# Performance work log

Measured on AMD Instinct MI355X. Metric: run time of the kernel, lower is better.

The kernel has to match this reference:

```python
import jax, jax.numpy as jnp
import numpy as np

EPS = 1e-12  # matches torch F.normalize default eps
WEIGHT = jnp.array([1.0, 1.0, 1.0], dtype=jnp.float32)  # per-channel loss weights


def _l2norm(x, axis):
    # torch F.normalize: x / max(||x||_2, eps)
    n = jnp.sqrt(jnp.sum(x * x, axis=axis, keepdims=True))
    return x / jnp.maximum(n, EPS)


def setup_inputs() -> dict:
    key = jax.random.key(0)
    k1, k2 = jax.random.split(key)
    shape = (16, 3, 512, 512)  # [B, C, H, W]
    return {
        "x": jax.random.normal(k1, shape, dtype=jnp.float32),
        "ref": jax.random.normal(k2, shape, dtype=jnp.float32),
    }


def reference(x, ref):
    # trace(rownorm(A) @ rownorm(B)^T) == sum(rownorm(A) * rownorm(B));
    # trace(colnorm(A)^T @ colnorm(B)) == sum(colnorm(A) * colnorm(B)).
    B, C, H, W = x.shape
    # per (batch, channel) traces, vectorized over all dims
    a = jnp.sum(_l2norm(x, -1) * _l2norm(ref, -1), axis=(-2, -1)) / H  # [B, C]
    b = jnp.sum(_l2norm(x, -2) * _l2norm(ref, -2), axis=(-2, -1)) / W  # [B, C]
    a = -jnp.sum(a * WEIGHT) / B
    b = -jnp.sum(b * WEIGHT) / B
    return a + b
```

## Files before the change

### kernel.cpp

```cpp
#include <hip/hip_runtime.h>

#define B_N 16
#define C_N 3
#define H_N 512
#define W_N 512
#define PLANES (B_N * C_N)
#define ROWS_PER_BLOCK 32
#define CHUNKS (H_N / ROWS_PER_BLOCK)
#define NBLK (PLANES * CHUNKS)
#define STATS3 (W_N * 3)
#define SCALE (-1.0f / 8192.0f)
#define EPS_F 1e-12f

__global__ __launch_bounds__(256) void spl_main_kernel(
    const float* __restrict__ x, const float* __restrict__ r,
    float* __restrict__ colpart, float* __restrict__ rowpart) {
    const int p     = blockIdx.x / CHUNKS;
    const int chunk = blockIdx.x % CHUNKS;
    const int wave  = threadIdx.x >> 6;
    const int lane  = threadIdx.x & 63;

    const float* xp = x + (size_t)p * (H_N * W_N);
    const float* rp = r + (size_t)p * (H_N * W_N);

    float cxx[8] = {0, 0, 0, 0, 0, 0, 0, 0};
    float crr[8] = {0, 0, 0, 0, 0, 0, 0, 0};
    float cxr[8] = {0, 0, 0, 0, 0, 0, 0, 0};
    float rowacc = 0.0f;

    const int r0 = chunk * ROWS_PER_BLOCK;
    for (int j = 0; j < ROWS_PER_BLOCK / 4; ++j) {
        const int row = r0 + wave + 4 * j;
        const float4* xr4 = (const float4*)(xp + (size_t)row * W_N);
        const float4* rr4 = (const float4*)(rp + (size_t)row * W_N);
        const float4 xa = xr4[lane];
        const float4 xb = xr4[lane + 64];
        const float4 ra = rr4[lane];
        const float4 rb = rr4[lane + 64];

        cxx[0] += xa.x * xa.x; cxx[1] += xa.y * xa.y; cxx[2] += xa.z * xa.z; cxx[3] += xa.w * xa.w;
        cxx[4] += xb.x * xb.x; cxx[5] += xb.y * xb.y; cxx[6] += xb.z * xb.z; cxx[7] += xb.w * xb.w;
        crr[0] += ra.x * ra.x; crr[1] += ra.y * ra.y; crr[2] += ra.z * ra.z; crr[3] += ra.w * ra.w;
        crr[4] += rb.x * rb.x; crr[5] += rb.y * rb.y; crr[6] += rb.z * rb.z; crr[7] += rb.w * rb.w;
        cxr[0] += xa.x * ra.x; cxr[1] += xa.y * ra.y; cxr[2] += xa.z * ra.z; cxr[3] += xa.w * ra.w;
        cxr[4] += xb.x * rb.x; cxr[5] += xb.y * rb.y; cxr[6] += xb.z * rb.z; cxr[7] += xb.w * rb.w;

        float sxx = cxx[0] + cxx[1] + cxx[2] + cxx[3] + cxx[4] + cxx[5] + cxx[6] + cxx[7];
        float srr = crr[0] + crr[1] + crr[2] + crr[3] + crr[4] + crr[5] + crr[6] + crr[7];
        float sxr = cxr[0] + cxr[1] + cxr[2] + cxr[3] + cxr[4] + cxr[5] + cxr[6] + cxr[7];
        sxx = xa.x * xa.x + xa.y * xa.y + xa.z * xa.z + xa.w * xa.w
            + xb.x * xb.x + xb.y * xb.y + xb.z * xb.z + xb.w * xb.w;
        srr = ra.x * ra.x + ra.y * ra.y + ra.z * ra.z + ra.w * ra.w
            + rb.x * rb.x + rb.y * rb.y + rb.z * rb.z + rb.w * rb.w;
        sxr = xa.x * ra.x + xa.y * ra.y + xa.z * ra.z + xa.w * ra.w
            + xb.x * rb.x + xb.y * rb.y + xb.z * rb.z + xb.w * rb.w;
        #pragma unroll
        for (int m = 32; m > 0; m >>= 1) {
            sxx += __shfl_down(sxx, m, 64);
            srr += __shfl_down(srr, m, 64);
            sxr += __shfl_down(sxr, m, 64);
        }
        if (lane == 0) {
            const float nx = fmaxf(sqrtf(sxx), EPS_F);
            const float nr = fmaxf(sqrtf(srr), EPS_F);
            rowacc += sxr / (nx * nr);
        }
    }

    __shared__ float smem[4][STATS3];
    #pragma unroll
    for (int k = 0; k < 4; ++k) {
        const int c0 = 4 * lane + k;
        const int c1 = c0 + 256;
        smem[wave][c0 * 3 + 0] = cxx[k];
        smem[wave][c0 * 3 + 1] = crr[k];
        smem[wave][c0 * 3 + 2] = cxr[k];
        smem[wave][c1 * 3 + 0] = cxx[4 + k];
        smem[wave][c1 * 3 + 1] = crr[4 + k];
        smem[wave][c1 * 3 + 2] = cxr[4 + k];
    }
    __shared__ float rowsums[4];
    if (lane == 0) rowsums[wave] = rowacc;
    __syncthreads();

    float* cp = colpart + (size_t)blockIdx.x * STATS3;
    #pragma unroll
    for (int k = 0; k < 6; ++k) {
        const int e = threadIdx.x + 256 * k;
        cp[e] = smem[0][e] + smem[1][e] + smem[2][e] + smem[3][e];
    }
    if (threadIdx.x == 0)
        rowpart[blockIdx.x] = rowsums[0] + rowsums[1] + rowsums[2] + rowsums[3];
}

__global__ __launch_bounds__(256) void spl_reduce_kernel(
    const float* __restrict__ colpart, const float* __restrict__ rowpart,
    float* __restrict__ planesum) {
    const int p = blockIdx.x;
    float acc[6] = {0, 0, 0, 0, 0, 0};
    const float* base = colpart + (size_t)p * CHUNKS * STATS3;
    for (int c = 0; c < CHUNKS; ++c) {
        const float* bc = base + c * STATS3;
        #pragma unroll
        for (int k = 0; k < 6; ++k) acc[k] += bc[threadIdx.x + 256 * k];
    }
    __shared__ float sums[STATS3];
    #pragma unroll
    for (int k = 0; k < 6; ++k) sums[threadIdx.x + 256 * k] = acc[k];
    __syncthreads();

    float term = 0.0f;
    #pragma unroll
    for (int k = 0; k < 2; ++k) {
        const int col = threadIdx.x + 256 * k;
        const float sxx = sums[col * 3 + 0];
        const float srr = sums[col * 3 + 1];
        const float sxr = sums[col * 3 + 2];
        term += sxr / (fmaxf(sqrtf(sxx), EPS_F) * fmaxf(sqrtf(srr), EPS_F));
    }
    if (threadIdx.x < CHUNKS) term += rowpart[p * CHUNKS + threadIdx.x];

    #pragma unroll
    for (int m = 32; m > 0; m >>= 1) term += __shfl_down(term, m, 64);
    __shared__ float ws[4];
    if ((threadIdx.x & 63) == 0) ws[threadIdx.x >> 6] = term;
    __syncthreads();
    if (threadIdx.x == 0) planesum[p] = ws[0] + ws[1] + ws[2] + ws[3];
}

__global__ void spl_final_kernel(const float* __restrict__ planesum,
                                 float* __restrict__ out) {
    float v = (threadIdx.x < PLANES) ? planesum[threadIdx.x] : 0.0f;
    #pragma unroll
    for (int m = 32; m > 0; m >>= 1) v += __shfl_down(v, m, 64);
    if (threadIdx.x == 0) out[0] = SCALE * v;
}

extern "C" void kernel_launch(void* const* d_in, const int* in_sizes, int n_in,
                              void* d_out, int out_size, void* d_ws, size_t ws_size,
                              hipStream_t stream) {
    const float* x   = (const float*)d_in[0];
    const float* ref = (const float*)d_in[1];
    float* out = (float*)d_out;

    float* colpart  = (float*)d_ws;
    float* rowpart  = colpart + (size_t)NBLK * STATS3;
    float* planesum = rowpart + NBLK;

    spl_main_kernel<<<NBLK, 256, 0, stream>>>(x, ref, colpart, rowpart);
    spl_reduce_kernel<<<PLANES, 256, 0, stream>>>(colpart, rowpart, planesum);
    spl_final_kernel<<<1, 64, 0, stream>>>(planesum, out);
}
```

Before: 119.9 us.

## Batch row reductions per wave and halve rows per block for more parallelism

Each wave now handles four consecutive rows with a fully unrolled loop, so all loads are issued up front. The cross-lane shuffle reductions for the four rows are interleaved after the loads instead of running after every row. Rows per block drop from 32 to 16, which doubles the block count and the colpart traffic written and read by the reduce kernel. The launch bound now asks for 6 blocks per SIMD, which may constrain registers.

Result: slower. 188.3 us (+57.0%).

```diff
diff --git a/kernel.cpp b/kernel.cpp
--- a/kernel.cpp
+++ b/kernel.cpp
@@ -5,14 +5,15 @@
 #define H_N 512
 #define W_N 512
 #define PLANES (B_N * C_N)
-#define ROWS_PER_BLOCK 32
+#define ROWS_PER_BLOCK 16
+#define ROWS_PER_WAVE 4
 #define CHUNKS (H_N / ROWS_PER_BLOCK)
 #define NBLK (PLANES * CHUNKS)
 #define STATS3 (W_N * 3)
 #define SCALE (-1.0f / 8192.0f)
 #define EPS_F 1e-12f
 
-__global__ __launch_bounds__(256) void spl_main_kernel(
+__global__ __launch_bounds__(256, 6) void spl_main_kernel(
     const float* __restrict__ x, const float* __restrict__ r,
     float* __restrict__ colpart, float* __restrict__ rowpart) {
     const int p     = blockIdx.x / CHUNKS;
@@ -26,11 +27,12 @@
     float cxx[8] = {0, 0, 0, 0, 0, 0, 0, 0};
     float crr[8] = {0, 0, 0, 0, 0, 0, 0, 0};
     float cxr[8] = {0, 0, 0, 0, 0, 0, 0, 0};
-    float rowacc = 0.0f;
+    float psxx[ROWS_PER_WAVE], psrr[ROWS_PER_WAVE], psxr[ROWS_PER_WAVE];
 
-    const int r0 = chunk * ROWS_PER_BLOCK;
-    for (int j = 0; j < ROWS_PER_BLOCK / 4; ++j) {
-        const int row = r0 + wave + 4 * j;
+    const int r0 = chunk * ROWS_PER_BLOCK + wave * ROWS_PER_WAVE;
+    #pragma unroll
+    for (int j = 0; j < ROWS_PER_WAVE; ++j) {
+        const int row = r0 + j;
         const float4* xr4 = (const float4*)(xp + (size_t)row * W_N);
         const float4* rr4 = (const float4*)(rp + (size_t)row * W_N);
         const float4 xa = xr4[lane];
@@ -38,32 +40,37 @@
         const float4 ra = rr4[lane];
         const float4 rb = rr4[lane + 64];
 
-        cxx[0] += xa.x * xa.x; cxx[1] += xa.y * xa.y; cxx[2] += xa.z * xa.z; cxx[3] += xa.w * xa.w;
-        cxx[4] += xb.x * xb.x; cxx[5] += xb.y * xb.y; cxx[6] += xb.z * xb.z; cxx[7] += xb.w * xb.w;
-        crr[0] += ra.x * ra.x; crr[1] += ra.y * ra.y; crr[2] += ra.z * ra.z; crr[3] += ra.w * ra.w;
-        crr[4] += rb.x * rb.x; crr[5] += rb.y * rb.y; crr[6] += rb.z * rb.z; crr[7] += rb.w * rb.w;
-        cxr[0] += xa.x * ra.x; cxr[1] += xa.y * ra.y; cxr[2] += xa.z * ra.z; cxr[3] += xa.w * ra.w;
-        cxr[4] += xb.x * rb.x; cxr[5] += xb.y * rb.y; cxr[6] += xb.z * rb.z; cxr[7] += xb.w * rb.w;
+        const float ax[8] = {xa.x, xa.y, xa.z, xa.w, xb.x, xb.y, xb.z, xb.w};
+        const float rx[8] = {ra.x, ra.y, ra.z, ra.w, rb.x, rb.y, rb.z, rb.w};
 
-        float sxx = cxx[0] + cxx[1] + cxx[2] + cxx[3] + cxx[4] + cxx[5] + cxx[6] + cxx[7];
-        float srr = crr[0] + crr[1] + crr[2] + crr[3] + crr[4] + crr[5] + crr[6] + crr[7];
-        float sxr = cxr[0] + cxr[1] + cxr[2] + cxr[3] + cxr[4] + cxr[5] + cxr[6] + cxr[7];
-        sxx = xa.x * xa.x + xa.y * xa.y + xa.z * xa.z + xa.w * xa.w
-            + xb.x * xb.x + xb.y * xb.y + xb.z * xb.z + xb.w * xb.w;
-        srr = ra.x * ra.x + ra.y * ra.y + ra.z * ra.z + ra.w * ra.w
-            + rb.x * rb.x + rb.y * rb.y + rb.z * rb.z + rb.w * rb.w;
-        sxr = xa.x * ra.x + xa.y * ra.y + xa.z * ra.z + xa.w * ra.w
-            + xb.x * rb.x + xb.y * rb.y + xb.z * rb.z + xb.w * rb.w;
+        float sxx = 0.0f, srr = 0.0f, sxr = 0.0f;
         #pragma unroll
-        for (int m = 32; m > 0; m >>= 1) {
-            sxx += __shfl_down(sxx, m, 64);
-            srr += __shfl_down(srr, m, 64);
-            sxr += __shfl_down(sxr, m, 64);
+        for (int k = 0; k < 8; ++k) {
+            const float txx = ax[k] * ax[k];
+            const float trr = rx[k] * rx[k];
+            const float txr = ax[k] * rx[k];
+            cxx[k] += txx; crr[k] += trr; cxr[k] += txr;
+            sxx += txx;    srr += trr;    sxr += txr;
         }
-        if (lane == 0) {
-            const float nx = fmaxf(sqrtf(sxx), EPS_F);
-            const float nr = fmaxf(sqrtf(srr), EPS_F);
-            rowacc += sxr / (nx * nr);
+        psxx[j] = sxx; psrr[j] = srr; psxr[j] = sxr;
+    }
+
+    #pragma unroll
+    for (int m = 32; m > 0; m >>= 1) {
+        #pragma unroll
+        for (int j = 0; j < ROWS_PER_WAVE; ++j) {
+            psxx[j] += __shfl_down(psxx[j], m, 64);
+            psrr[j] += __shfl_down(psrr[j], m, 64);
+            psxr[j] += __shfl_down(psxr[j], m, 64);
+        }
+    }
+    float rowacc = 0.0f;
+    if (lane == 0) {
+        #pragma unroll
+        for (int j = 0; j < ROWS_PER_WAVE; ++j) {
+            const float nx = fmaxf(sqrtf(psxx[j]), EPS_F);
+            const float nr = fmaxf(sqrtf(psrr[j]), EPS_F);
+            rowacc += psxr[j] / (nx * nr);
         }
     }
 
```
